# Kernel optimization log

Measured on AMD Instinct MI355X. Metric: run time of the kernel, lower is better.

Reference implementation:

```python
import jax, jax.numpy as jnp
import numpy as np
from jax import lax

EPS = 1e-5


def _conv(x, w, b, stride, pad):
    # x: [B,C,H,W], w: [O,I,kh,kw] (NCHW / OIHW, same as torch Conv2d)
    y = lax.conv_general_dilated(
        x, w, window_strides=stride,
        padding=[(pad[0], pad[0]), (pad[1], pad[1])],
        dimension_numbers=('NCHW', 'OIHW', 'NCHW'))
    return y + b[None, :, None, None]


def _bn(x, gamma, beta, mean, var):
    # BatchNorm2d in eval mode (running statistics)
    inv = gamma / jnp.sqrt(var + EPS)
    return x * inv[None, :, None, None] + (beta - mean * inv)[None, :, None, None]


def _mask_time(x, lens):
    # Vectorized replacement of the per-sample narrow/fill loop:
    # zero every time step >= lens[b] along the last axis.
    t = jnp.arange(x.shape[3])
    keep = (t[None, :] < lens[:, None]).astype(x.dtype)  # [B, W]
    return x * keep[:, None, None, :]


def _new_len(lens, kernel_w, stride_w, pad_w):
    # matches get_new_sequence_lengths for Conv2d with dilation 1
    return (lens + 2 * pad_w - (kernel_w - 1) - 1) // stride_w + 1


def _forward(inputs, seq_lengths,
             w1, b1, g1, be1, m1, v1,
             w2, b2, g2, be2, m2, v2):
    lens = seq_lengths.astype(jnp.int32)
    # layer 1: Conv2d(1,32,(41,11),(2,2),(20,5))
    x = _conv(inputs, w1, b1, (2, 2), (20, 5))
    lens = _new_len(lens, 11, 2, 5)
    x = _mask_time(x, lens)
    # BatchNorm2d(32) -> mask
    x = _mask_time(_bn(x, g1, be1, m1, v1), lens)
    # Hardtanh(0,20) -> mask
    x = _mask_time(jnp.clip(x, 0.0, 20.0), lens)
    # layer 2: Conv2d(32,32,(21,11),(2,1),(10,5))
    x = _conv(x, w2, b2, (2, 1), (10, 5))
    lens = _new_len(lens, 11, 1, 5)
    x = _mask_time(x, lens)
    x = _mask_time(_bn(x, g2, be2, m2, v2), lens)
    x = _mask_time(jnp.clip(x, 0.0, 20.0), lens)
    return x, lens


def setup_inputs() -> dict:
    key = jax.random.key(0)
    ks = jax.random.split(key, 8)
    inputs = jax.random.normal(ks[0], (32, 1, 161, 1024), dtype=jnp.float32)
    seq_lengths = jax.random.randint(ks[1], (32,), 1, 1024, dtype=jnp.int32)
    w1 = jax.random.normal(ks[2], (32, 1, 41, 11), dtype=jnp.float32) * 0.05
    b1 = jax.random.normal(ks[3], (32,), dtype=jnp.float32) * 0.05
    w2 = jax.random.normal(ks[4], (32, 32, 21, 11), dtype=jnp.float32) * 0.02
    b2 = jax.random.normal(ks[5], (32,), dtype=jnp.float32) * 0.05
    g1 = jnp.ones((32,), jnp.float32)
    be1 = jnp.zeros((32,), jnp.float32)
    m1 = jax.random.normal(ks[6], (32,), dtype=jnp.float32) * 0.1
    v1 = jnp.ones((32,), jnp.float32)
    g2 = jnp.ones((32,), jnp.float32)
    be2 = jnp.zeros((32,), jnp.float32)
    m2 = jax.random.normal(ks[7], (32,), dtype=jnp.float32) * 0.1
    v2 = jnp.ones((32,), jnp.float32)
    return {"inputs": inputs, "seq_lengths": seq_lengths,
            "w1": w1, "b1": b1, "g1": g1, "be1": be1, "m1": m1, "v1": v1,
            "w2": w2, "b2": b2, "g2": g2, "be2": be2, "m2": m2, "v2": v2}


def reference(inputs, seq_lengths, w1, b1, g1, be1, m1, v1,
              w2, b2, g2, be2, m2, v2):
    return _forward(inputs, seq_lengths, w1, b1, g1, be1, m1, v1,
                    w2, b2, g2, be2, m2, v2)
```

## Files before the change

kernel.cpp:

```cpp
#include <hip/hip_runtime.h>
#include <math.h>

#define B_    32
#define H_IN  161
#define W_IN  1024
#define C1_   32
#define H1_   81
#define W1_   512
#define C2_   32
#define H2_   41
#define W2_   512

#define OUT_X_SZ ((size_t)B_ * C2_ * H2_ * W2_)

#define WF2_B    0u
#define WF1_B    473088u
#define SCSH_B   515072u
#define LENS1_B  515584u
#define XG_B     515712u

#define WF2_N    236544
#define WF1_N    20992

typedef __bf16 v8bf __attribute__((ext_vector_type(8)));
typedef float v16f __attribute__((ext_vector_type(16)));

static __device__ __forceinline__ unsigned short f2bf(float f) {
    unsigned int u = __float_as_uint(f);
    unsigned int r = (u + 0x7fffu + ((u >> 16) & 1u)) >> 16;
    return (unsigned short)r;
}

__global__ void prep_kernel(const float* __restrict__ w1, const float* __restrict__ b1,
                            const float* __restrict__ g1, const float* __restrict__ be1,
                            const float* __restrict__ m1, const float* __restrict__ v1,
                            const float* __restrict__ w2, const float* __restrict__ b2,
                            const float* __restrict__ g2, const float* __restrict__ be2,
                            const float* __restrict__ m2, const float* __restrict__ v2,
                            const int* __restrict__ lens,
                            unsigned short* __restrict__ wf1, unsigned short* __restrict__ wf2,
                            float* __restrict__ scsh, int* __restrict__ lens1,
                            float* __restrict__ out_lens)
{
    const int i = blockIdx.x * blockDim.x + threadIdx.x;
    const int stride = gridDim.x * blockDim.x;

    for (int idx = i; idx < WF2_N; idx += stride) {
        int j  = idx & 7;
        int l  = (idx >> 3) & 63;
        int f  = idx >> 9;
        int ch = f & 1;
        int kwkh = f >> 1;
        int kw = kwkh % 11;
        int kh = kwkh / 11;
        int oc = l & 31;
        int c  = ch * 16 + ((l >> 5) << 3) + j;
        wf2[idx] = f2bf(w2[((oc * 32 + c) * 21 + kh) * 11 + kw]);
    }
    for (int idx = i; idx < WF1_N; idx += stride) {
        int j  = idx & 7;
        int l  = (idx >> 3) & 63;
        int kh = idx >> 9;
        int k  = ((l >> 5) << 3) + j;
        int oc = l & 31;
        wf1[idx] = (k < 11) ? f2bf(w1[oc * 451 + kh * 11 + k]) : (unsigned short)0;
    }
    if (i < 32) {
        float s1 = g1[i] / sqrtf(v1[i] + 1e-5f);
        scsh[i]      = s1;
        scsh[32 + i] = b1[i] * s1 + be1[i] - m1[i] * s1;
        float s2 = g2[i] / sqrtf(v2[i] + 1e-5f);
        scsh[64 + i] = s2;
        scsh[96 + i] = b2[i] * s2 + be2[i] - m2[i] * s2;
        int l1 = (lens[i] - 1) / 2 + 1;
        if (l1 > W1_) l1 = W1_;
        lens1[i] = l1;
        out_lens[i] = (float)l1;
    }
}

__global__ __launch_bounds__(256) void conv1_mfma(
    const float* __restrict__ x,
    const unsigned short* __restrict__ wf1,
    const float* __restrict__ scsh,
    const int* __restrict__ lens1,
    unsigned short* __restrict__ xg)
{
    const int t    = threadIdx.x;
    const int lane = t & 63;
    const int l31  = lane & 31;
    const int lhi  = lane >> 5;
    const int wv   = t >> 6;
    const int w0   = blockIdx.x * 256;
    const int h    = blockIdx.y;
    const int b    = blockIdx.z;

    __shared__ unsigned int srow[2][264];

    v16f acc0, acc1;
#pragma unroll
    for (int i = 0; i < 16; ++i) { acc0[i] = 0.f; acc1[i] = 0.f; }

    const int r0 = 2 * h - 20;
    const int cb = 2 * w0 - 5;
    const float* xb = x + (size_t)b * (H_IN * W_IN);

    const int dwbase = wv * 64 + l31 + 4 * lhi;

    {
        float a0 = 0.f, a1 = 0.f, c0v = 0.f, c1v = 0.f;
        if (r0 >= 0 && r0 < H_IN) {
            const float* src = xb + (size_t)r0 * W_IN;
            int c0 = cb + 2 * t;
            if ((unsigned)c0 < (unsigned)W_IN)       a0 = src[c0];
            if ((unsigned)(c0 + 1) < (unsigned)W_IN) a1 = src[c0 + 1];
            if (t < 7) {
                int c1 = cb + 2 * (256 + t);
                if ((unsigned)c1 < (unsigned)W_IN)       c0v = src[c1];
                if ((unsigned)(c1 + 1) < (unsigned)W_IN) c1v = src[c1 + 1];
            }
        }
        srow[0][t] = (unsigned int)f2bf(a0) | ((unsigned int)f2bf(a1) << 16);
        if (t < 7)
            srow[0][256 + t] = (unsigned int)f2bf(c0v) | ((unsigned int)f2bf(c1v) << 16);
    }
    __syncthreads();

    for (int kh = 0; kh < 41; ++kh) {
        const int p = kh & 1;
        const int rn = r0 + kh + 1;
        const bool rv = (kh < 40) && (rn >= 0) && (rn < H_IN);

        float a0 = 0.f, a1 = 0.f, c0v = 0.f, c1v = 0.f;
        if (rv) {
            const float* src = xb + (size_t)rn * W_IN;
            int c0 = cb + 2 * t;
            if ((unsigned)c0 < (unsigned)W_IN)       a0 = src[c0];
            if ((unsigned)(c0 + 1) < (unsigned)W_IN) a1 = src[c0 + 1];
            if (t < 7) {
                int c1 = cb + 2 * (256 + t);
                if ((unsigned)c1 < (unsigned)W_IN)       c0v = src[c1];
                if ((unsigned)(c1 + 1) < (unsigned)W_IN) c1v = src[c1 + 1];
            }
        }

        const int r = r0 + kh;
        if (r >= 0 && r < H_IN) {
            uint4 a_u = *((const uint4*)wf1 + kh * 32 + lane);
            v8bf a = __builtin_bit_cast(v8bf, a_u);
            const unsigned int* bp = &srow[p][0];
            {
                int dw = dwbase;
                uint4 bu;
                bu.x = bp[dw]; bu.y = bp[dw + 1]; bu.z = bp[dw + 2]; bu.w = bp[dw + 3];
                v8bf bb = __builtin_bit_cast(v8bf, bu);
                acc0 = __builtin_amdgcn_mfma_f32_32x32x16_bf16(a, bb, acc0, 0, 0, 0);
            }
            {
                int dw = dwbase + 32;
                uint4 bu;
                bu.x = bp[dw]; bu.y = bp[dw + 1]; bu.z = bp[dw + 2]; bu.w = bp[dw + 3];
                v8bf bb = __builtin_bit_cast(v8bf, bu);
                acc1 = __builtin_amdgcn_mfma_f32_32x32x16_bf16(a, bb, acc1, 0, 0, 0);
            }
        }

        if (rv) {
            srow[p ^ 1][t] = (unsigned int)f2bf(a0) | ((unsigned int)f2bf(a1) << 16);
            if (t < 7)
                srow[p ^ 1][256 + t] = (unsigned int)f2bf(c0v) | ((unsigned int)f2bf(c1v) << 16);
        }
        __syncthreads();
    }

    const int l1 = lens1[b];
#pragma unroll
    for (int nt = 0; nt < 2; ++nt) {
        const int w = w0 + wv * 64 + nt * 32 + l31;
        const bool keep = (w < l1);
        unsigned short* dp = xg + (((size_t)b * H1_ + h) * W1_ + w) * 32;
#pragma unroll
        for (int rq = 0; rq < 4; ++rq) {
            unsigned int wd[2];
#pragma unroll
            for (int d = 0; d < 2; ++d) {
                int rg = rq * 4 + d * 2;
                int oc = 8 * rq + 4 * lhi + d * 2;
                float av0 = (nt == 0) ? acc0[rg]     : acc1[rg];
                float av1 = (nt == 0) ? acc0[rg + 1] : acc1[rg + 1];
                float v0 = fminf(fmaxf(fmaf(av0, scsh[oc],     scsh[32 + oc]), 0.f), 20.f);
                float v1 = fminf(fmaxf(fmaf(av1, scsh[oc + 1], scsh[33 + oc]), 0.f), 20.f);
                if (!keep) { v0 = 0.f; v1 = 0.f; }
                wd[d] = (unsigned int)f2bf(v0) | ((unsigned int)f2bf(v1) << 16);
            }
            uint2 u; u.x = wd[0]; u.y = wd[1];
            *(uint2*)(dp + 8 * rq + 4 * lhi) = u;
        }
    }
}

#define ROWB 21280

__global__ __launch_bounds__(256, 3) void conv2_mfma(
    const unsigned short* __restrict__ xg,
    const unsigned short* __restrict__ wf2,
    const float* __restrict__ scsh,
    const int* __restrict__ lens1,
    float* __restrict__ out)
{
    const int t    = threadIdx.x;
    const int lane = t & 63;
    const int l31  = lane & 31;
    const int lhi  = lane >> 5;
    const int wv   = t >> 6;
    const int w0B  = blockIdx.x * 256;
    const int h    = blockIdx.y;
    const int b    = blockIdx.z;

    __shared__ __align__(16) char sbuf[2 * ROWB];

    v16f acc0, acc1;
#pragma unroll
    for (int i = 0; i < 16; ++i) { acc0[i] = 0.f; acc1[i] = 0.f; }

    const int st_lds = (t >> 2) * 80 + (t & 3) * 16;
    const int rd_lds = (wv * 64 + l31) * 80 + lhi * 16;

    const unsigned short* xb = xg + (size_t)b * (H1_ * W1_ * 32);
    const int r0 = 2 * h - 10;

    {
        int r = r0;
        if (r >= 0 && r < H1_) {
            const unsigned short* xrow = xb + (size_t)r * (W1_ * 32);
#pragma unroll
            for (int it = 0; it < 5; ++it) {
                int i = t + it * 256;
                int wp = (i >> 2) + w0B - 5;
                uint4 z; z.x = z.y = z.z = z.w = 0u;
                if (i < 1064 && wp >= 0 && wp < W1_)
                    z = *(const uint4*)(xrow + (size_t)wp * 32 + (i & 3) * 8);
                if (i < 1064)
                    *(uint4*)(sbuf + st_lds + it * 5120) = z;
            }
        }
    }
    __syncthreads();

    for (int kh = 0; kh < 21; ++kh) {
        const int p = kh & 1;
        const int rn = r0 + kh + 1;
        const bool stage_next = (kh < 20) && (rn >= 0) && (rn < H1_);

        uint4 g0, g1, g2, g3, g4;
        g0.x=g0.y=g0.z=g0.w=0u; g1=g0; g2=g0; g3=g0; g4=g0;
        if (stage_next) {
            const unsigned short* xrow = xb + (size_t)rn * (W1_ * 32);
            const int wbase = (t >> 2) + w0B - 5;
            const int ck = (t & 3) * 8;
            if (wbase >= 0 && wbase < W1_)                 g0 = *(const uint4*)(xrow + (size_t)wbase * 32 + ck);
            if (wbase + 64 >= 0 && wbase + 64 < W1_)       g1 = *(const uint4*)(xrow + (size_t)(wbase + 64) * 32 + ck);
            if (wbase + 128 < W1_)                         g2 = *(const uint4*)(xrow + (size_t)(wbase + 128) * 32 + ck);
            if (wbase + 192 < W1_)                         g3 = *(const uint4*)(xrow + (size_t)(wbase + 192) * 32 + ck);
            if (t < 40 && wbase + 256 < W1_)               g4 = *(const uint4*)(xrow + (size_t)(wbase + 256) * 32 + ck);
        }

        const int r = r0 + kh;
        if (r >= 0 && r < H1_) {
            const unsigned short* wkh = wf2 + kh * (22 * 512);
            const char* bbase = sbuf + p * ROWB + rd_lds;
#pragma unroll
            for (int kw = 0; kw < 11; ++kw) {
#pragma unroll
                for (int ch = 0; ch < 2; ++ch) {
                    uint4 a_u = *((const uint4*)(wkh + ((kw * 2 + ch) << 9)) + lane);
                    uint4 b0_u = *(const uint4*)(bbase + kw * 80 + ch * 32);
                    uint4 b1_u = *(const uint4*)(bbase + 2560 + kw * 80 + ch * 32);
                    v8bf a  = __builtin_bit_cast(v8bf, a_u);
                    v8bf bb0 = __builtin_bit_cast(v8bf, b0_u);
                    v8bf bb1 = __builtin_bit_cast(v8bf, b1_u);
                    acc0 = __builtin_amdgcn_mfma_f32_32x32x16_bf16(a, bb0, acc0, 0, 0, 0);
                    acc1 = __builtin_amdgcn_mfma_f32_32x32x16_bf16(a, bb1, acc1, 0, 0, 0);
                }
            }
        }

        if (stage_next) {
            char* wb = sbuf + (p ^ 1) * ROWB + st_lds;
            *(uint4*)(wb)            = g0;
            *(uint4*)(wb + 5120)     = g1;
            *(uint4*)(wb + 2 * 5120) = g2;
            *(uint4*)(wb + 3 * 5120) = g3;
            if (t < 40) *(uint4*)(wb + 4 * 5120) = g4;
        }
        __syncthreads();
    }

    const int l2 = lens1[b];
#pragma unroll
    for (int nt = 0; nt < 2; ++nt) {
        const int w = w0B + wv * 64 + nt * 32 + l31;
        const bool keep = (w < l2);
#pragma unroll
        for (int reg = 0; reg < 16; ++reg) {
            int oc = (reg & 3) + 8 * (reg >> 2) + 4 * lhi;
            float av = (nt == 0) ? acc0[reg] : acc1[reg];
            float v = fmaf(av, scsh[64 + oc], scsh[96 + oc]);
            v = fminf(fmaxf(v, 0.f), 20.f);
            out[(((size_t)b * C2_ + oc) * H2_ + h) * W2_ + w] = keep ? v : 0.f;
        }
    }
}

extern "C" void kernel_launch(void* const* d_in, const int* in_sizes, int n_in,
                              void* d_out, int out_size, void* d_ws, size_t ws_size,
                              hipStream_t stream) {
    const float* inputs = (const float*)d_in[0];
    const int*   slen   = (const int*)d_in[1];
    const float* w1 = (const float*)d_in[2];
    const float* b1 = (const float*)d_in[3];
    const float* g1 = (const float*)d_in[4];
    const float* be1 = (const float*)d_in[5];
    const float* m1 = (const float*)d_in[6];
    const float* v1 = (const float*)d_in[7];
    const float* w2 = (const float*)d_in[8];
    const float* b2 = (const float*)d_in[9];
    const float* g2 = (const float*)d_in[10];
    const float* be2 = (const float*)d_in[11];
    const float* m2 = (const float*)d_in[12];
    const float* v2 = (const float*)d_in[13];

    char* ws = (char*)d_ws;
    unsigned short* wf2  = (unsigned short*)(ws + WF2_B);
    unsigned short* wf1  = (unsigned short*)(ws + WF1_B);
    float*          scsh = (float*)(ws + SCSH_B);
    int*            lens1 = (int*)(ws + LENS1_B);
    unsigned short* xg   = (unsigned short*)(ws + XG_B);

    float* out_x    = (float*)d_out;
    float* out_lens = out_x + OUT_X_SZ;

    hipLaunchKernelGGL(prep_kernel, dim3(256), dim3(256), 0, stream,
                       w1, b1, g1, be1, m1, v1, w2, b2, g2, be2, m2, v2,
                       slen, wf1, wf2, scsh, lens1, out_lens);

    hipLaunchKernelGGL(conv1_mfma, dim3(2, H1_, B_), dim3(256), 0, stream,
                       inputs, wf1, scsh, lens1, xg);

    hipLaunchKernelGGL(conv2_mfma, dim3(2, H2_, B_), dim3(256), 0, stream,
                       xg, wf2, scsh, lens1, out_x);
}
```

Baseline: 548.5 us.

## Compute two output rows per conv2 block to reuse staged input rows

Restructures conv2 so each 128-thread block computes two adjacent output rows over 256 width positions. Each staged input row in LDS then feeds both output rows, which roughly halves global input traffic and LDS staging per output. Each wave now holds a 4x2 tile of 32x32 accumulators to raise register reuse of B operands. The change also adds an XOR-swizzled LDS layout against bank conflicts, a remapped flat block ID for L2 locality, and s_setprio around the MFMA loop. The costs are higher register pressure (128 accumulator floats per lane) and fewer threads per block.

```diff
diff --git a/kernel.cpp b/kernel.cpp
--- a/kernel.cpp
+++ b/kernel.cpp
@@ -199,9 +199,9 @@
     }
 }
 
-#define ROWB 21280
-
-__global__ __launch_bounds__(256, 3) void conv2_mfma(
+#define C2BUF 17024
+
+__global__ __launch_bounds__(128, 2) void conv2_mfma(
     const unsigned short* __restrict__ xg,
     const unsigned short* __restrict__ wf2,
     const float* __restrict__ scsh,
@@ -212,102 +212,148 @@
     const int lane = t & 63;
     const int l31  = lane & 31;
     const int lhi  = lane >> 5;
-    const int wv   = t >> 6;
-    const int w0B  = blockIdx.x * 256;
-    const int h    = blockIdx.y;
-    const int b    = blockIdx.z;
-
-    __shared__ __align__(16) char sbuf[2 * ROWB];
-
-    v16f acc0, acc1;
-#pragma unroll
-    for (int i = 0; i < 16; ++i) { acc0[i] = 0.f; acc1[i] = 0.f; }
-
-    const int st_lds = (t >> 2) * 80 + (t & 3) * 16;
-    const int rd_lds = (wv * 64 + l31) * 80 + lhi * 16;
-
+    const int wid  = t >> 6;
+
+    const int id   = blockIdx.x;
+    const int sid  = (id & 7) * 168 + (id >> 3);
+    const int wblk = sid & 1;
+    const int bh   = sid >> 1;
+    const int hp   = bh % 21;
+    const int b    = bh / 21;
+    const int h0   = hp << 1;
+    const bool h1v = (h0 + 1) < 41;
+
+    __shared__ __align__(16) char sbuf[2 * C2BUF];
+
+    const int w0B = wblk << 8;
     const unsigned short* xb = xg + (size_t)b * (H1_ * W1_ * 32);
-    const int r0 = 2 * h - 10;
-
-    {
-        int r = r0;
-        if (r >= 0 && r < H1_) {
-            const unsigned short* xrow = xb + (size_t)r * (W1_ * 32);
-#pragma unroll
-            for (int it = 0; it < 5; ++it) {
-                int i = t + it * 256;
-                int wp = (i >> 2) + w0B - 5;
-                uint4 z; z.x = z.y = z.z = z.w = 0u;
-                if (i < 1064 && wp >= 0 && wp < W1_)
-                    z = *(const uint4*)(xrow + (size_t)wp * 32 + (i & 3) * 8);
-                if (i < 1064)
-                    *(uint4*)(sbuf + st_lds + it * 5120) = z;
-            }
-        }
-    }
+
+    int srcoff[9], ldsoff[9];
+    bool vld[9];
+#pragma unroll
+    for (int i = 0; i < 9; ++i) {
+        int k   = t + i * 128;
+        int pos = k >> 2;
+        int sg  = k & 3;
+        int wp  = w0B + pos - 5;
+        vld[i]    = (k < 1064) && (wp >= 0) && (wp < W1_);
+        srcoff[i] = wp * 64 + sg * 16;
+        ldsoff[i] = pos * 64 + ((sg ^ ((pos >> 1) & 3)) << 4);
+    }
+
+    const int rlo = max(0, 2 * h0 - 10);
+    const int rhi = min(80, 2 * h0 + 12);
+
+    v16f acc[2][4];
+#pragma unroll
+    for (int hh = 0; hh < 2; ++hh)
+#pragma unroll
+        for (int mt = 0; mt < 4; ++mt)
+#pragma unroll
+            for (int q = 0; q < 16; ++q) acc[hh][mt][q] = 0.f;
+
+    uint4 g[9];
+
+#define C2_STAGE_LOAD(ROW)                                                   \
+    {                                                                        \
+        const char* xrow = (const char*)(xb + (size_t)(ROW) * (W1_ * 32));   \
+        _Pragma("unroll")                                                    \
+        for (int i = 0; i < 9; ++i) {                                        \
+            g[i].x = g[i].y = g[i].z = g[i].w = 0u;                          \
+            if (vld[i]) g[i] = *(const uint4*)(xrow + srcoff[i]);            \
+        }                                                                    \
+    }
+
+#define C2_STAGE_WRITE(PP)                                                   \
+    {                                                                        \
+        char* dst = sbuf + (PP) * C2BUF;                                     \
+        _Pragma("unroll")                                                    \
+        for (int i = 0; i < 8; ++i) *(uint4*)(dst + ldsoff[i]) = g[i];       \
+        if (t < 40) *(uint4*)(dst + ldsoff[8]) = g[8];                       \
+    }
+
+    C2_STAGE_LOAD(rlo);
+    C2_STAGE_WRITE(0);
     __syncthreads();
 
-    for (int kh = 0; kh < 21; ++kh) {
-        const int p = kh & 1;
-        const int rn = r0 + kh + 1;
-        const bool stage_next = (kh < 20) && (rn >= 0) && (rn < H1_);
-
-        uint4 g0, g1, g2, g3, g4;
-        g0.x=g0.y=g0.z=g0.w=0u; g1=g0; g2=g0; g3=g0; g4=g0;
-        if (stage_next) {
-            const unsigned short* xrow = xb + (size_t)rn * (W1_ * 32);
-            const int wbase = (t >> 2) + w0B - 5;
-            const int ck = (t & 3) * 8;
-            if (wbase >= 0 && wbase < W1_)                 g0 = *(const uint4*)(xrow + (size_t)wbase * 32 + ck);
-            if (wbase + 64 >= 0 && wbase + 64 < W1_)       g1 = *(const uint4*)(xrow + (size_t)(wbase + 64) * 32 + ck);
-            if (wbase + 128 < W1_)                         g2 = *(const uint4*)(xrow + (size_t)(wbase + 128) * 32 + ck);
-            if (wbase + 192 < W1_)                         g3 = *(const uint4*)(xrow + (size_t)(wbase + 192) * 32 + ck);
-            if (t < 40 && wbase + 256 < W1_)               g4 = *(const uint4*)(xrow + (size_t)(wbase + 256) * 32 + ck);
-        }
-
-        const int r = r0 + kh;
-        if (r >= 0 && r < H1_) {
-            const unsigned short* wkh = wf2 + kh * (22 * 512);
-            const char* bbase = sbuf + p * ROWB + rd_lds;
-#pragma unroll
-            for (int kw = 0; kw < 11; ++kw) {
-#pragma unroll
-                for (int ch = 0; ch < 2; ++ch) {
-                    uint4 a_u = *((const uint4*)(wkh + ((kw * 2 + ch) << 9)) + lane);
-                    uint4 b0_u = *(const uint4*)(bbase + kw * 80 + ch * 32);
-                    uint4 b1_u = *(const uint4*)(bbase + 2560 + kw * 80 + ch * 32);
-                    v8bf a  = __builtin_bit_cast(v8bf, a_u);
-                    v8bf bb0 = __builtin_bit_cast(v8bf, b0_u);
-                    v8bf bb1 = __builtin_bit_cast(v8bf, b1_u);
-                    acc0 = __builtin_amdgcn_mfma_f32_32x32x16_bf16(a, bb0, acc0, 0, 0, 0);
-                    acc1 = __builtin_amdgcn_mfma_f32_32x32x16_bf16(a, bb1, acc1, 0, 0, 0);
-                }
-            }
-        }
-
-        if (stage_next) {
-            char* wb = sbuf + (p ^ 1) * ROWB + st_lds;
-            *(uint4*)(wb)            = g0;
-            *(uint4*)(wb + 5120)     = g1;
-            *(uint4*)(wb + 2 * 5120) = g2;
-            *(uint4*)(wb + 3 * 5120) = g3;
-            if (t < 40) *(uint4*)(wb + 4 * 5120) = g4;
-        }
+    const uint4* wq = (const uint4*)wf2;
+    const int pbase = (wid << 7) + l31;
+
+    for (int r = rlo; r <= rhi; ++r) {
+        const int p = (r - rlo) & 1;
+
+        if (r < rhi) C2_STAGE_LOAD(r + 1);
+
+        const int kh0 = r + 10 - 2 * h0;
+        const int kh1 = kh0 - 2;
+        const bool vh0 = (kh0 <= 20);
+        const bool vh1 = h1v && (kh1 >= 0);
+        const int f0 = kh0 * 22;
+        const int f1 = kh1 * 22;
+        const char* bb = sbuf + p * C2BUF;
+
+        __builtin_amdgcn_s_setprio(1);
+#pragma unroll
+        for (int kw = 0; kw < 11; ++kw) {
+            const int pos0 = pbase + kw;
+            const int swz  = (pos0 >> 1) & 3;
+            const int a0   = (pos0 << 6) + ((lhi ^ swz) << 4);
+            const int a1   = a0 ^ 32;
+            uint4 b00 = *(const uint4*)(bb + a0);
+            uint4 b01 = *(const uint4*)(bb + a0 + 2048);
+            uint4 b02 = *(const uint4*)(bb + a0 + 4096);
+            uint4 b03 = *(const uint4*)(bb + a0 + 6144);
+            uint4 b10 = *(const uint4*)(bb + a1);
+            uint4 b11 = *(const uint4*)(bb + a1 + 2048);
+            uint4 b12 = *(const uint4*)(bb + a1 + 4096);
+            uint4 b13 = *(const uint4*)(bb + a1 + 6144);
+            if (vh0) {
+                v8bf A0 = __builtin_bit_cast(v8bf, wq[(f0 + 2 * kw) * 64 + lane]);
+                v8bf A1 = __builtin_bit_cast(v8bf, wq[(f0 + 2 * kw + 1) * 64 + lane]);
+                acc[0][0] = __builtin_amdgcn_mfma_f32_32x32x16_bf16(A0, __builtin_bit_cast(v8bf, b00), acc[0][0], 0, 0, 0);
+                acc[0][1] = __builtin_amdgcn_mfma_f32_32x32x16_bf16(A0, __builtin_bit_cast(v8bf, b01), acc[0][1], 0, 0, 0);
+                acc[0][2] = __builtin_amdgcn_mfma_f32_32x32x16_bf16(A0, __builtin_bit_cast(v8bf, b02), acc[0][2], 0, 0, 0);
+                acc[0][3] = __builtin_amdgcn_mfma_f32_32x32x16_bf16(A0, __builtin_bit_cast(v8bf, b03), acc[0][3], 0, 0, 0);
+                acc[0][0] = __builtin_amdgcn_mfma_f32_32x32x16_bf16(A1, __builtin_bit_cast(v8bf, b10), acc[0][0], 0, 0, 0);
+                acc[0][1] = __builtin_amdgcn_mfma_f32_32x32x16_bf16(A1, __builtin_bit_cast(v8bf, b11), acc[0][1], 0, 0, 0);
+                acc[0][2] = __builtin_amdgcn_mfma_f32_32x32x16_bf16(A1, __builtin_bit_cast(v8bf, b12), acc[0][2], 0, 0, 0);
+                acc[0][3] = __builtin_amdgcn_mfma_f32_32x32x16_bf16(A1, __builtin_bit_cast(v8bf, b13), acc[0][3], 0, 0, 0);
+            }
+            if (vh1) {
+                v8bf C0 = __builtin_bit_cast(v8bf, wq[(f1 + 2 * kw) * 64 + lane]);
+                v8bf C1 = __builtin_bit_cast(v8bf, wq[(f1 + 2 * kw + 1) * 64 + lane]);
+                acc[1][0] = __builtin_amdgcn_mfma_f32_32x32x16_bf16(C0, __builtin_bit_cast(v8bf, b00), acc[1][0], 0, 0, 0);
+                acc[1][1] = __builtin_amdgcn_mfma_f32_32x32x16_bf16(C0, __builtin_bit_cast(v8bf, b01), acc[1][1], 0, 0, 0);
+                acc[1][2] = __builtin_amdgcn_mfma_f32_32x32x16_bf16(C0, __builtin_bit_cast(v8bf, b02), acc[1][2], 0, 0, 0);
+                acc[1][3] = __builtin_amdgcn_mfma_f32_32x32x16_bf16(C0, __builtin_bit_cast(v8bf, b03), acc[1][3], 0, 0, 0);
+                acc[1][0] = __builtin_amdgcn_mfma_f32_32x32x16_bf16(C1, __builtin_bit_cast(v8bf, b10), acc[1][0], 0, 0, 0);
+                acc[1][1] = __builtin_amdgcn_mfma_f32_32x32x16_bf16(C1, __builtin_bit_cast(v8bf, b11), acc[1][1], 0, 0, 0);
+                acc[1][2] = __builtin_amdgcn_mfma_f32_32x32x16_bf16(C1, __builtin_bit_cast(v8bf, b12), acc[1][2], 0, 0, 0);
+                acc[1][3] = __builtin_amdgcn_mfma_f32_32x32x16_bf16(C1, __builtin_bit_cast(v8bf, b13), acc[1][3], 0, 0, 0);
+            }
+        }
+        __builtin_amdgcn_s_setprio(0);
+
+        if (r < rhi) C2_STAGE_WRITE(p ^ 1);
         __syncthreads();
     }
 
     const int l2 = lens1[b];
 #pragma unroll
-    for (int nt = 0; nt < 2; ++nt) {
-        const int w = w0B + wv * 64 + nt * 32 + l31;
-        const bool keep = (w < l2);
-#pragma unroll
-        for (int reg = 0; reg < 16; ++reg) {
-            int oc = (reg & 3) + 8 * (reg >> 2) + 4 * lhi;
-            float av = (nt == 0) ? acc0[reg] : acc1[reg];
-            float v = fmaf(av, scsh[64 + oc], scsh[96 + oc]);
-            v = fminf(fmaxf(v, 0.f), 20.f);
-            out[(((size_t)b * C2_ + oc) * H2_ + h) * W2_ + w] = keep ? v : 0.f;
+    for (int hh = 0; hh < 2; ++hh) {
+        if (hh == 1 && !h1v) break;
+        const int h = h0 + hh;
+#pragma unroll
+        for (int mt = 0; mt < 4; ++mt) {
+            const int w = w0B + (wid << 7) + (mt << 5) + l31;
+            const bool keep = (w < l2);
+#pragma unroll
+            for (int reg = 0; reg < 16; ++reg) {
+                const int oc = (reg & 3) + 8 * (reg >> 2) + 4 * lhi;
+                float v = fmaf(acc[hh][mt][reg], scsh[64 + oc], scsh[96 + oc]);
+                v = fminf(fmaxf(v, 0.f), 20.f);
+                out[(((size_t)b * C2_ + oc) * H2_ + h) * W2_ + w] = keep ? v : 0.f;
+            }
         }
     }
 }
@@ -347,6 +393,6 @@
     hipLaunchKernelGGL(conv1_mfma, dim3(2, H1_, B_), dim3(256), 0, stream,
                        inputs, wf1, scsh, lens1, xg);
 
-    hipLaunchKernelGGL(conv2_mfma, dim3(2, H2_, B_), dim3(256), 0, stream,
+    hipLaunchKernelGGL(conv2_mfma, dim3(1344), dim3(128), 0, stream,
                        xg, wf2, scsh, lens1, out_x);
 }
```

After: 607.9 us. +10.8%, slower.

## Compute two output rows per block in both convs to reuse staged input rows

Applied to the files above, without the earlier changes.

Each block of both conv kernels now computes two adjacent output rows. The staged input row is shared by both through weight tensors padded with two zero rows of kernel height, so every row loaded into LDS feeds twice as many MFMAs. This halves the number of blocks and the redundant global row loads, since vertical stride 2 means neighbouring output rows overlap heavily in input rows. Conv2 also gets a swizzled 1D block index and raises wave priority around its MFMA loop. The cost is more accumulator registers (four 16-float accumulators per thread), which may lower occupancy, plus some MFMAs wasted on the zero-padded weight rows.

```diff
diff --git a/kernel.cpp b/kernel.cpp
--- a/kernel.cpp
+++ b/kernel.cpp
@@ -14,13 +14,13 @@
 #define OUT_X_SZ ((size_t)B_ * C2_ * H2_ * W2_)
 
 #define WF2_B    0u
-#define WF1_B    473088u
-#define SCSH_B   515072u
-#define LENS1_B  515584u
-#define XG_B     515712u
-
-#define WF2_N    236544
-#define WF1_N    20992
+#define WF1_B    563200u
+#define SCSH_B   609280u
+#define LENS1_B  609792u
+#define XG_B     609920u
+
+#define WF2_N    281600
+#define WF1_N    23040
 
 typedef __bf16 v8bf __attribute__((ext_vector_type(8)));
 typedef float v16f __attribute__((ext_vector_type(16)));
@@ -51,19 +51,23 @@
         int f  = idx >> 9;
         int ch = f & 1;
         int kwkh = f >> 1;
-        int kw = kwkh % 11;
-        int kh = kwkh / 11;
+        int kw  = kwkh % 11;
+        int khp = kwkh / 11;
+        int kh  = khp - 2;
         int oc = l & 31;
         int c  = ch * 16 + ((l >> 5) << 3) + j;
-        wf2[idx] = f2bf(w2[((oc * 32 + c) * 21 + kh) * 11 + kw]);
+        wf2[idx] = (kh >= 0 && kh < 21)
+                 ? f2bf(w2[((oc * 32 + c) * 21 + kh) * 11 + kw]) : (unsigned short)0;
     }
     for (int idx = i; idx < WF1_N; idx += stride) {
-        int j  = idx & 7;
-        int l  = (idx >> 3) & 63;
-        int kh = idx >> 9;
-        int k  = ((l >> 5) << 3) + j;
-        int oc = l & 31;
-        wf1[idx] = (k < 11) ? f2bf(w1[oc * 451 + kh * 11 + k]) : (unsigned short)0;
+        int j   = idx & 7;
+        int l   = (idx >> 3) & 63;
+        int khp = idx >> 9;
+        int kh  = khp - 2;
+        int k   = ((l >> 5) << 3) + j;
+        int oc  = l & 31;
+        wf1[idx] = (k < 11 && kh >= 0 && kh < 41)
+                 ? f2bf(w1[oc * 451 + kh * 11 + k]) : (unsigned short)0;
     }
     if (i < 32) {
         float s1 = g1[i] / sqrtf(v1[i] + 1e-5f);
@@ -92,16 +96,22 @@
     const int lhi  = lane >> 5;
     const int wv   = t >> 6;
     const int w0   = blockIdx.x * 256;
-    const int h    = blockIdx.y;
+    const int hp   = blockIdx.y;
     const int b    = blockIdx.z;
+    const int h0   = hp * 2;
+    const bool h1ok = (h0 + 1) < H1_;
 
     __shared__ unsigned int srow[2][264];
 
-    v16f acc0, acc1;
-#pragma unroll
-    for (int i = 0; i < 16; ++i) { acc0[i] = 0.f; acc1[i] = 0.f; }
-
-    const int r0 = 2 * h - 20;
+    v16f acc[2][2];
+#pragma unroll
+    for (int hh = 0; hh < 2; ++hh)
+#pragma unroll
+        for (int nt = 0; nt < 2; ++nt)
+#pragma unroll
+            for (int q = 0; q < 16; ++q) acc[hh][nt][q] = 0.f;
+
+    const int r0 = 2 * h0 - 20;
     const int cb = 2 * w0 - 5;
     const float* xb = x + (size_t)b * (H_IN * W_IN);
 
@@ -126,10 +136,12 @@
     }
     __syncthreads();
 
-    for (int kh = 0; kh < 41; ++kh) {
-        const int p = kh & 1;
-        const int rn = r0 + kh + 1;
-        const bool rv = (kh < 40) && (rn >= 0) && (rn < H_IN);
+    const uint4* wf1q = (const uint4*)wf1;
+
+    for (int kp = 0; kp < 43; ++kp) {
+        const int p = kp & 1;
+        const int rn = r0 + kp + 1;
+        const bool rv = (kp < 42) && (rn >= 0) && (rn < H_IN);
 
         float a0 = 0.f, a1 = 0.f, c0v = 0.f, c1v = 0.f;
         if (rv) {
@@ -144,25 +156,26 @@
             }
         }
 
-        const int r = r0 + kh;
+        const int r = r0 + kp;
         if (r >= 0 && r < H_IN) {
-            uint4 a_u = *((const uint4*)wf1 + kh * 32 + lane);
-            v8bf a = __builtin_bit_cast(v8bf, a_u);
+            uint4 a0u = wf1q[(kp + 2) * 32 + lane];
+            uint4 a1u = wf1q[kp * 32 + lane];
+            v8bf A0 = __builtin_bit_cast(v8bf, a0u);
+            v8bf A1 = __builtin_bit_cast(v8bf, a1u);
             const unsigned int* bp = &srow[p][0];
+            uint4 bu0, bu1;
             {
                 int dw = dwbase;
-                uint4 bu;
-                bu.x = bp[dw]; bu.y = bp[dw + 1]; bu.z = bp[dw + 2]; bu.w = bp[dw + 3];
-                v8bf bb = __builtin_bit_cast(v8bf, bu);
-                acc0 = __builtin_amdgcn_mfma_f32_32x32x16_bf16(a, bb, acc0, 0, 0, 0);
-            }
-            {
-                int dw = dwbase + 32;
-                uint4 bu;
-                bu.x = bp[dw]; bu.y = bp[dw + 1]; bu.z = bp[dw + 2]; bu.w = bp[dw + 3];
-                v8bf bb = __builtin_bit_cast(v8bf, bu);
-                acc1 = __builtin_amdgcn_mfma_f32_32x32x16_bf16(a, bb, acc1, 0, 0, 0);
-            }
+                bu0.x = bp[dw]; bu0.y = bp[dw + 1]; bu0.z = bp[dw + 2]; bu0.w = bp[dw + 3];
+                dw += 32;
+                bu1.x = bp[dw]; bu1.y = bp[dw + 1]; bu1.z = bp[dw + 2]; bu1.w = bp[dw + 3];
+            }
+            v8bf B0 = __builtin_bit_cast(v8bf, bu0);
+            v8bf B1 = __builtin_bit_cast(v8bf, bu1);
+            acc[0][0] = __builtin_amdgcn_mfma_f32_32x32x16_bf16(A0, B0, acc[0][0], 0, 0, 0);
+            acc[0][1] = __builtin_amdgcn_mfma_f32_32x32x16_bf16(A0, B1, acc[0][1], 0, 0, 0);
+            acc[1][0] = __builtin_amdgcn_mfma_f32_32x32x16_bf16(A1, B0, acc[1][0], 0, 0, 0);
+            acc[1][1] = __builtin_amdgcn_mfma_f32_32x32x16_bf16(A1, B1, acc[1][1], 0, 0, 0);
         }
 
         if (rv) {
@@ -175,26 +188,31 @@
 
     const int l1 = lens1[b];
 #pragma unroll
-    for (int nt = 0; nt < 2; ++nt) {
-        const int w = w0 + wv * 64 + nt * 32 + l31;
-        const bool keep = (w < l1);
-        unsigned short* dp = xg + (((size_t)b * H1_ + h) * W1_ + w) * 32;
-#pragma unroll
-        for (int rq = 0; rq < 4; ++rq) {
-            unsigned int wd[2];
-#pragma unroll
-            for (int d = 0; d < 2; ++d) {
-                int rg = rq * 4 + d * 2;
-                int oc = 8 * rq + 4 * lhi + d * 2;
-                float av0 = (nt == 0) ? acc0[rg]     : acc1[rg];
-                float av1 = (nt == 0) ? acc0[rg + 1] : acc1[rg + 1];
-                float v0 = fminf(fmaxf(fmaf(av0, scsh[oc],     scsh[32 + oc]), 0.f), 20.f);
-                float v1 = fminf(fmaxf(fmaf(av1, scsh[oc + 1], scsh[33 + oc]), 0.f), 20.f);
-                if (!keep) { v0 = 0.f; v1 = 0.f; }
-                wd[d] = (unsigned int)f2bf(v0) | ((unsigned int)f2bf(v1) << 16);
-            }
-            uint2 u; u.x = wd[0]; u.y = wd[1];
-            *(uint2*)(dp + 8 * rq + 4 * lhi) = u;
+    for (int hh = 0; hh < 2; ++hh) {
+        if (hh == 1 && !h1ok) break;
+        const int h = h0 + hh;
+#pragma unroll
+        for (int nt = 0; nt < 2; ++nt) {
+            const int w = w0 + wv * 64 + nt * 32 + l31;
+            const bool keep = (w < l1);
+            unsigned short* dp = xg + (((size_t)b * H1_ + h) * W1_ + w) * 32;
+#pragma unroll
+            for (int rq = 0; rq < 4; ++rq) {
+                unsigned int wd[2];
+#pragma unroll
+                for (int d = 0; d < 2; ++d) {
+                    int rg = rq * 4 + d * 2;
+                    int oc = 8 * rq + 4 * lhi + d * 2;
+                    float av0 = acc[hh][nt][rg];
+                    float av1 = acc[hh][nt][rg + 1];
+                    float v0 = fminf(fmaxf(fmaf(av0, scsh[oc],     scsh[32 + oc]), 0.f), 20.f);
+                    float v1 = fminf(fmaxf(fmaf(av1, scsh[oc + 1], scsh[33 + oc]), 0.f), 20.f);
+                    if (!keep) { v0 = 0.f; v1 = 0.f; }
+                    wd[d] = (unsigned int)f2bf(v0) | ((unsigned int)f2bf(v1) << 16);
+                }
+                uint2 u; u.x = wd[0]; u.y = wd[1];
+                *(uint2*)(dp + 8 * rq + 4 * lhi) = u;
+            }
         }
     }
 }
@@ -213,21 +231,32 @@
     const int l31  = lane & 31;
     const int lhi  = lane >> 5;
     const int wv   = t >> 6;
-    const int w0B  = blockIdx.x * 256;
-    const int h    = blockIdx.y;
-    const int b    = blockIdx.z;
+
+    const int id   = blockIdx.x;
+    const int sid  = (id & 7) * 168 + (id >> 3);
+    const int wblk = sid & 1;
+    const int bh   = sid >> 1;
+    const int hp   = bh % 21;
+    const int b    = bh / 21;
+    const int h0   = hp * 2;
+    const bool h1ok = (h0 + 1) < H2_;
+    const int w0B  = wblk << 8;
 
     __shared__ __align__(16) char sbuf[2 * ROWB];
 
-    v16f acc0, acc1;
-#pragma unroll
-    for (int i = 0; i < 16; ++i) { acc0[i] = 0.f; acc1[i] = 0.f; }
+    v16f acc[2][2];
+#pragma unroll
+    for (int hh = 0; hh < 2; ++hh)
+#pragma unroll
+        for (int nt = 0; nt < 2; ++nt)
+#pragma unroll
+            for (int q = 0; q < 16; ++q) acc[hh][nt][q] = 0.f;
 
     const int st_lds = (t >> 2) * 80 + (t & 3) * 16;
     const int rd_lds = (wv * 64 + l31) * 80 + lhi * 16;
 
     const unsigned short* xb = xg + (size_t)b * (H1_ * W1_ * 32);
-    const int r0 = 2 * h - 10;
+    const int r0 = 2 * h0 - 10;
 
     {
         int r = r0;
@@ -247,10 +276,12 @@
     }
     __syncthreads();
 
-    for (int kh = 0; kh < 21; ++kh) {
-        const int p = kh & 1;
-        const int rn = r0 + kh + 1;
-        const bool stage_next = (kh < 20) && (rn >= 0) && (rn < H1_);
+    const uint4* wq = (const uint4*)wf2;
+
+    for (int kp = 0; kp < 23; ++kp) {
+        const int p = kp & 1;
+        const int rn = r0 + kp + 1;
+        const bool stage_next = (kp < 22) && (rn >= 0) && (rn < H1_);
 
         uint4 g0, g1, g2, g3, g4;
         g0.x=g0.y=g0.z=g0.w=0u; g1=g0; g2=g0; g3=g0; g4=g0;
@@ -265,24 +296,31 @@
             if (t < 40 && wbase + 256 < W1_)               g4 = *(const uint4*)(xrow + (size_t)(wbase + 256) * 32 + ck);
         }
 
-        const int r = r0 + kh;
+        const int r = r0 + kp;
         if (r >= 0 && r < H1_) {
-            const unsigned short* wkh = wf2 + kh * (22 * 512);
+            const int f0 = (kp + 2) * 22;
+            const int f1 = kp * 22;
             const char* bbase = sbuf + p * ROWB + rd_lds;
+            __builtin_amdgcn_s_setprio(1);
 #pragma unroll
             for (int kw = 0; kw < 11; ++kw) {
 #pragma unroll
                 for (int ch = 0; ch < 2; ++ch) {
-                    uint4 a_u = *((const uint4*)(wkh + ((kw * 2 + ch) << 9)) + lane);
-                    uint4 b0_u = *(const uint4*)(bbase + kw * 80 + ch * 32);
-                    uint4 b1_u = *(const uint4*)(bbase + 2560 + kw * 80 + ch * 32);
-                    v8bf a  = __builtin_bit_cast(v8bf, a_u);
-                    v8bf bb0 = __builtin_bit_cast(v8bf, b0_u);
-                    v8bf bb1 = __builtin_bit_cast(v8bf, b1_u);
-                    acc0 = __builtin_amdgcn_mfma_f32_32x32x16_bf16(a, bb0, acc0, 0, 0, 0);
-                    acc1 = __builtin_amdgcn_mfma_f32_32x32x16_bf16(a, bb1, acc1, 0, 0, 0);
+                    uint4 a0u = wq[(f0 + kw * 2 + ch) * 64 + lane];
+                    uint4 a1u = wq[(f1 + kw * 2 + ch) * 64 + lane];
+                    uint4 b0u = *(const uint4*)(bbase + kw * 80 + ch * 32);
+                    uint4 b1u = *(const uint4*)(bbase + 2560 + kw * 80 + ch * 32);
+                    v8bf A0 = __builtin_bit_cast(v8bf, a0u);
+                    v8bf A1 = __builtin_bit_cast(v8bf, a1u);
+                    v8bf B0 = __builtin_bit_cast(v8bf, b0u);
+                    v8bf B1 = __builtin_bit_cast(v8bf, b1u);
+                    acc[0][0] = __builtin_amdgcn_mfma_f32_32x32x16_bf16(A0, B0, acc[0][0], 0, 0, 0);
+                    acc[0][1] = __builtin_amdgcn_mfma_f32_32x32x16_bf16(A0, B1, acc[0][1], 0, 0, 0);
+                    acc[1][0] = __builtin_amdgcn_mfma_f32_32x32x16_bf16(A1, B0, acc[1][0], 0, 0, 0);
+                    acc[1][1] = __builtin_amdgcn_mfma_f32_32x32x16_bf16(A1, B1, acc[1][1], 0, 0, 0);
                 }
             }
+            __builtin_amdgcn_s_setprio(0);
         }
 
         if (stage_next) {
@@ -298,16 +336,20 @@
 
     const int l2 = lens1[b];
 #pragma unroll
-    for (int nt = 0; nt < 2; ++nt) {
-        const int w = w0B + wv * 64 + nt * 32 + l31;
-        const bool keep = (w < l2);
-#pragma unroll
-        for (int reg = 0; reg < 16; ++reg) {
-            int oc = (reg & 3) + 8 * (reg >> 2) + 4 * lhi;
-            float av = (nt == 0) ? acc0[reg] : acc1[reg];
-            float v = fmaf(av, scsh[64 + oc], scsh[96 + oc]);
-            v = fminf(fmaxf(v, 0.f), 20.f);
-            out[(((size_t)b * C2_ + oc) * H2_ + h) * W2_ + w] = keep ? v : 0.f;
+    for (int hh = 0; hh < 2; ++hh) {
+        if (hh == 1 && !h1ok) break;
+        const int h = h0 + hh;
+#pragma unroll
+        for (int nt = 0; nt < 2; ++nt) {
+            const int w = w0B + wv * 64 + nt * 32 + l31;
+            const bool keep = (w < l2);
+#pragma unroll
+            for (int reg = 0; reg < 16; ++reg) {
+                const int oc = (reg & 3) + 8 * (reg >> 2) + 4 * lhi;
+                float v = fmaf(acc[hh][nt][reg], scsh[64 + oc], scsh[96 + oc]);
+                v = fminf(fmaxf(v, 0.f), 20.f);
+                out[(((size_t)b * C2_ + oc) * H2_ + h) * W2_ + w] = keep ? v : 0.f;
+            }
         }
     }
 }
@@ -344,9 +386,9 @@
                        w1, b1, g1, be1, m1, v1, w2, b2, g2, be2, m2, v2,
                        slen, wf1, wf2, scsh, lens1, out_lens);
 
-    hipLaunchKernelGGL(conv1_mfma, dim3(2, H1_, B_), dim3(256), 0, stream,
+    hipLaunchKernelGGL(conv1_mfma, dim3(2, 41, B_), dim3(256), 0, stream,
                        inputs, wf1, scsh, lens1, xg);
 
-    hipLaunchKernelGGL(conv2_mfma, dim3(2, H2_, B_), dim3(256), 0, stream,
+    hipLaunchKernelGGL(conv2_mfma, dim3(1344), dim3(256), 0, stream,
                        xg, wf2, scsh, lens1, out_x);
 }
```

New measurement: 533.9 us. -2.7%, faster.
